# Performance work log

Hardware: AMD Instinct MI355X
Metric: run time of the kernel (lower is better)

## Reference

```python
import jax, jax.numpy as jnp
import numpy as np

GAMMAK = 1.0 / 256.0  # 1/(2*d) so kernel values don't underflow for unit-gaussian data


def setup_inputs() -> dict:
    key = jax.random.key(0)
    k1, k2, k3, k4, k5 = jax.random.split(key, 5)
    N, d = 8192, 128
    X = jax.random.normal(k1, (N, d), dtype=jnp.float32)
    y = jax.random.normal(k2, (N - 1, d), dtype=jnp.float32)
    y_next = jax.random.normal(k3, (N - 1, d), dtype=jnp.float32)
    # reset_transform initializes R=eye, t=0; perturb slightly for nontrivial math
    R = jnp.eye(d, dtype=jnp.float32) + 0.01 * jax.random.normal(k4, (d, d), dtype=jnp.float32)
    t = 0.01 * jax.random.normal(k5, (d, 1), dtype=jnp.float32)
    return {"X": X, "y": y, "y_next": y_next, "R": R, "t": t}


def reference(X, y, y_next, R, t):
    # _transform_pts: (R @ y.T + t).T == y @ R.T + t.squeeze()
    yt = y @ R.T + t[:, 0]            # (N-1, d)
    Xb = X[:-1]                        # (N-1, d) kernel base points
    # pairwise_sqeuclidean(Xb, yt), clamped at 0
    sq = jnp.clip(
        jnp.sum(Xb * Xb, axis=1)[:, None]
        + jnp.sum(yt * yt, axis=1)[None, :]
        - 2.0 * (Xb @ yt.T),
        0.0, None,
    )                                  # (N-1, N-1)
    G = jnp.exp(-GAMMAK * sq)
    # diag(1/rowsum) @ G  ==  G / rowsum[:, None]  (avoids explicit NxN diagonal)
    y_pred = (G / jnp.sum(G, axis=1, keepdims=True)) @ X[1:]  # (N-1, d)
    return y_pred
```

## Files before the change

### kernel.cpp

```cpp
#include <hip/hip_runtime.h>
#include <hip/hip_bf16.h>


#define LOG2E 1.44269504088896340736f
#define KNEG (-(1.0f/256.0f)*LOG2E)
#define KA2C (2.0f*(1.0f/256.0f)*LOG2E)

typedef __attribute__((ext_vector_type(4)))  float f32x4;
typedef __attribute__((ext_vector_type(16))) float f32x16;
typedef __attribute__((ext_vector_type(8)))  short bf16x8;

__device__ __forceinline__ unsigned short f2bf(float f) {
  unsigned u = __builtin_bit_cast(unsigned, f);
  u = (u + 0x7fffu + ((u >> 16) & 1u)) >> 16;
  return (unsigned short)u;
}
__device__ __forceinline__ unsigned pk2bf(float a, float b) {
  __hip_bfloat162 h = __float22bfloat162_rn(float2{a, b});
  unsigned u;
  __builtin_memcpy(&u, &h, 4);
  return u;
}
__device__ __forceinline__ bf16x8 pack8(float4 p0, float4 p1) {
  uint4 u;
  u.x = pk2bf(p0.x, p0.y); u.y = pk2bf(p0.z, p0.w);
  u.z = pk2bf(p1.x, p1.y); u.w = pk2bf(p1.z, p1.w);
  return __builtin_bit_cast(bf16x8, u);
}
__device__ __forceinline__ float fast_exp2(float x) {
#if __has_builtin(__builtin_amdgcn_exp2f)
  return __builtin_amdgcn_exp2f(x);
#else
  return exp2f(x);
#endif
}
__device__ __forceinline__ void gl2lds16(const void* g, void* l) {
  __builtin_amdgcn_global_load_lds((const __attribute__((address_space(1))) unsigned int*)g,
                                   (__attribute__((address_space(3))) unsigned int*)l, 16, 0, 0);
}
__device__ __forceinline__ f32x16 mfma_32x32x16(bf16x8 a, bf16x8 b, f32x16 c) {
  return __builtin_amdgcn_mfma_f32_32x32x16_bf16(a, b, c, 0, 0, 0);
}

#define T_STRIDE 34816
#define V_OFF    18432

__global__ __launch_bounds__(256) void k_prep(const float* __restrict__ y,
                                              const float* __restrict__ R,
                                              const float* __restrict__ t,
                                              const float* __restrict__ X,
                                              unsigned short* __restrict__ ctp) {
  __shared__ union {
    struct { unsigned short ytt[128 * 132]; float ynl[128]; } yb;
    float xt[65 * 132];
  } sm;
  const int tid = threadIdx.x;

  if (blockIdx.x < 64) {
    const int wv = tid >> 6, ln = tid & 63;
    const int l = ln & 31, h = ln >> 5;
    const int B = blockIdx.x;
    const int rw = B * 128 + wv * 32;

    bf16x8 af[8];
    {
      int row = rw + l; if (row > 8190) row = 8190;
      const float* yr = y + (size_t)row * 128;
#pragma unroll
      for (int kc = 0; kc < 8; ++kc) {
        float4 p0 = *(const float4*)(yr + kc*16 + 8*h);
        float4 p1 = *(const float4*)(yr + kc*16 + 8*h + 4);
        af[kc] = pack8(p0, p1);
      }
    }
    f32x16 acc[4];
#pragma unroll
    for (int cc=0; cc<4; ++cc)
#pragma unroll
      for (int i=0;i<16;++i) acc[cc][i] = 0.f;
#pragma unroll
    for (int cc=0; cc<4; ++cc) {
      const float* Rr = R + (size_t)(cc*32 + l) * 128;
#pragma unroll
      for (int kc=0; kc<8; ++kc) {
        float4 p0 = *(const float4*)(Rr + kc*16 + 8*h);
        float4 p1 = *(const float4*)(Rr + kc*16 + 8*h + 4);
        acc[cc] = mfma_32x32x16(af[kc], pack8(p0, p1), acc[cc]);
      }
    }
    float tv0 = t[l], tv1 = t[32+l], tv2 = t[64+l], tv3 = t[96+l];
    float v0[16], v1[16], v2[16], v3[16], ssq[16];
#pragma unroll
    for (int r=0;r<16;++r) {
      v0[r]=acc[0][r]+tv0; v1[r]=acc[1][r]+tv1; v2[r]=acc[2][r]+tv2; v3[r]=acc[3][r]+tv3;
      ssq[r] = v0[r]*v0[r] + v1[r]*v1[r] + v2[r]*v2[r] + v3[r]*v3[r];
    }
#pragma unroll
    for (int off=1; off<32; off<<=1)
#pragma unroll
      for (int r=0;r<16;++r) ssq[r] += __shfl_xor(ssq[r], off, 64);
    if (l < 16) {
      int r = l;
      int rloc = wv*32 + (r&3) + 8*(r>>2) + 4*h;
      int grow = rw + (r&3) + 8*(r>>2) + 4*h;
      sm.yb.ynl[rloc] = (grow >= 8191) ? -1.0e4f : KNEG * ssq[r];
    }
#pragma unroll
    for (int r=0;r<16;++r) {
      int rloc = wv*32 + (r&3) + 8*(r>>2) + 4*h;
      sm.yb.ytt[rloc*132 +   0 + l] = f2bf(KA2C * v0[r]);
      sm.yb.ytt[rloc*132 +  32 + l] = f2bf(KA2C * v1[r]);
      sm.yb.ytt[rloc*132 +  64 + l] = f2bf(KA2C * v2[r]);
      sm.yb.ytt[rloc*132 +  96 + l] = f2bf(KA2C * v3[r]);
    }
    __syncthreads();
    const int Tt = B*2 + (wv>>1);
    const int jcw = wv & 1;
    char* base = (char*)ctp + (size_t)Tt*T_STRIDE;
#pragma unroll
    for (int kc=0;kc<8;++kc) {
      const unsigned short* s = &sm.yb.ytt[(wv*32 + l)*132 + kc*16 + 8*h];
      uint2 a = *(const uint2*)(s);
      uint2 b = *(const uint2*)(s + 4);
      uint4 o; o.x=a.x; o.y=a.y; o.z=b.x; o.w=b.y;
      *(uint4*)(base + (jcw*9 + kc)*1024 + ln*16) = o;
    }
    {
      float yn = sm.yb.ynl[wv*32 + l];
      unsigned short hi = f2bf(yn);
      float hif = __builtin_bit_cast(float, (unsigned)hi << 16);
      unsigned short lo = f2bf(yn - hif);
      uint4 o; o.x = (h == 0) ? ((unsigned)hi | ((unsigned)lo << 16)) : 0u;
      o.y = 0u; o.z = 0u; o.w = 0u;
      *(uint4*)(base + (jcw*9 + 8)*1024 + ln*16) = o;
    }
  } else {
    const int T = blockIdx.x - 64;
    const int jt = T * 64;
    {
      int rr = tid >> 2, q4 = tid & 3;
      int row = jt + rr; if (row > 8191) row = 8191;
      const float* src = X + (size_t)row*128 + q4*32;
      float* dst = &sm.xt[rr*132 + q4*32];
#pragma unroll
      for (int i=0;i<8;++i) *(float4*)(dst + i*4) = *(const float4*)(src + i*4);
      if (tid < 4) {
        int row2 = jt + 64; if (row2 > 8191) row2 = 8191;
        const float* s2 = X + (size_t)row2*128 + tid*32;
        float* d2 = &sm.xt[64*132 + tid*32];
#pragma unroll
        for (int i=0;i<8;++i) *(float4*)(d2 + i*4) = *(const float4*)(s2 + i*4);
      }
    }
    __syncthreads();
    char* base = (char*)ctp + (size_t)T*T_STRIDE + V_OFF;
#pragma unroll
    for (int it=0; it<4; ++it) {
      int E = tid + it*256;
      int lp = E & 63, grp = E >> 6;
      int cc = grp & 3, jc16 = grp >> 2;
      int jb = jc16*16 + 8*(lp>>5);
      int c  = cc*32 + (lp & 31);
      uint4 o;
      o.x = pk2bf(sm.xt[(jb+1)*132 + c], sm.xt[(jb+2)*132 + c]);
      o.y = pk2bf(sm.xt[(jb+3)*132 + c], sm.xt[(jb+4)*132 + c]);
      o.z = pk2bf(sm.xt[(jb+5)*132 + c], sm.xt[(jb+6)*132 + c]);
      o.w = pk2bf(sm.xt[(jb+7)*132 + c], sm.xt[(jb+8)*132 + c]);
      *(uint4*)(base + E*16) = o;
    }
  }
}

__global__ __launch_bounds__(256, 3) void k_main(
    const float* __restrict__ X,
    const unsigned short* __restrict__ ctp,
    float* __restrict__ accp,
    float* __restrict__ rsp,
    int js) {
  __shared__ unsigned short stg[T_STRIDE/2];
  __shared__ unsigned short gls[4*32*68];
  const int tid = threadIdx.x;
  const int wv = tid >> 6, ln = tid & 63;
  const int l = ln & 31, h = ln >> 5;
  const int row = blockIdx.x*128 + wv*32 + l;

  bf16x8 qf[9];
  {
    const float* xr = X + (size_t)row * 128;
#pragma unroll
    for (int kc=0;kc<8;++kc) {
      float4 p0 = *(const float4*)(xr + kc*16 + 8*h);
      float4 p1 = *(const float4*)(xr + kc*16 + 8*h + 4);
      qf[kc] = pack8(p0, p1);
    }
    uint4 o; o.x = (h == 0) ? 0x3F803F80u : 0u; o.y = 0u; o.z = 0u; o.w = 0u;
    qf[8] = __builtin_bit_cast(bf16x8, o);
  }
  f32x16 acc[4];
#pragma unroll
  for (int cc=0;cc<4;++cc)
#pragma unroll
    for (int i=0;i<16;++i) acc[cc][i]=0.f;
  float rs = 0.f;
  const int sp = blockIdx.y;
  const int Tbeg = (sp * 128) / js;
  const int Tend = ((sp + 1) * 128) / js;
  for (int T = Tbeg; T < Tend; ++T) {
    __syncthreads();
    {
      const char* cb = (const char*)ctp + (size_t)T*T_STRIDE;
#pragma unroll
      for (int i=0;i<9;++i) {
        int c = wv + 4*i;
        if (c < 34) gl2lds16(cb + c*1024 + ln*16, (char*)stg + c*1024);
      }
    }
    __syncthreads();
#pragma unroll
    for (int jc=0; jc<2; ++jc) {
      f32x16 sa;
#pragma unroll
      for (int i=0;i<16;++i) sa[i]=0.f;
#pragma unroll
      for (int kc=0;kc<9;++kc) {
        bf16x8 a = *(const bf16x8*)((const char*)stg + (jc*9+kc)*1024 + ln*16);
        sa = mfma_32x32x16(a, qf[kc], sa);
      }
#pragma unroll
      for (int rg=0; rg<4; ++rg) {
        float g0 = fast_exp2(sa[rg*4+0]);
        float g1 = fast_exp2(sa[rg*4+1]);
        float g2 = fast_exp2(sa[rg*4+2]);
        float g3 = fast_exp2(sa[rg*4+3]);
        rs += (g0+g1) + (g2+g3);
        uint2 w; w.x = pk2bf(g0, g1); w.y = pk2bf(g2, g3);
        int j0 = jc*32 + 8*rg + 4*h;
        *(uint2*)&gls[(wv*32+l)*68 + j0] = w;
      }
      __builtin_amdgcn_wave_barrier();
#pragma unroll
      for (int jj=0; jj<2; ++jj) {
        int jc16 = jc*2 + jj;
        const unsigned short* gp = &gls[(wv*32+l)*68 + jc16*16 + 8*h];
        uint2 g0 = *(const uint2*)(gp);
        uint2 g1 = *(const uint2*)(gp + 4);
        uint4 gv; gv.x=g0.x; gv.y=g0.y; gv.z=g1.x; gv.w=g1.y;
        bf16x8 pb = __builtin_bit_cast(bf16x8, gv);
#pragma unroll
        for (int cc=0;cc<4;++cc) {
          bf16x8 a2 = *(const bf16x8*)((const char*)stg + V_OFF + (jc16*4+cc)*1024 + ln*16);
          acc[cc] = mfma_32x32x16(a2, pb, acc[cc]);
        }
      }
      __builtin_amdgcn_wave_barrier();
    }
  }
  rs += __shfl_xor(rs, 32, 64);
  if (h == 0) rsp[(size_t)sp*8192 + row] = rs;
#pragma unroll
  for (int cc=0;cc<4;++cc)
#pragma unroll
    for (int r=0;r<16;++r) {
      int c = cc*32 + (r&3) + 8*(r>>2) + 4*h;
      accp[((size_t)sp*128 + c)*8192 + row] = acc[cc][r];
    }
}

__global__ __launch_bounds__(256) void k_fin(const float* __restrict__ accp,
                                             const float* __restrict__ rsp,
                                             float* __restrict__ out,
                                             int js) {
  __shared__ float tr[64*132];
  __shared__ float rinv[64];
  const int tid = threadIdx.x;
  const int r0 = blockIdx.x * 64;
  if (tid < 64) {
    float s = 0.f;
    for (int sp=0; sp<js; ++sp) s += rsp[(size_t)sp*8192 + r0 + tid];
    rinv[tid] = 1.f / s;
  }
  const int rq = tid & 15, cg = tid >> 4;
  float v[8][4];
#pragma unroll
  for (int cc=0;cc<8;++cc)
#pragma unroll
    for (int k=0;k<4;++k) v[cc][k]=0.f;
  for (int sp=0; sp<js; ++sp) {
    const float* base = accp + ((size_t)sp*128 + cg*8)*8192 + r0 + rq*4;
#pragma unroll
    for (int cc=0; cc<8; ++cc) {
      float4 p = *(const float4*)(base + (size_t)cc*8192);
      v[cc][0]+=p.x; v[cc][1]+=p.y; v[cc][2]+=p.z; v[cc][3]+=p.w;
    }
  }
  __syncthreads();
#pragma unroll
  for (int cc=0;cc<8;++cc)
#pragma unroll
    for (int k=0;k<4;++k)
      tr[(rq*4+k)*132 + cg*8+cc] = v[cc][k] * rinv[rq*4+k];
  __syncthreads();
  {
    int r = tid >> 2, q = tid & 3;
    int grow = r0 + r;
    if (grow < 8191) {
      float* dst = out + (size_t)grow*128 + q*32;
      const float* s2 = &tr[r*132 + q*32];
#pragma unroll
      for (int i=0;i<8;++i) *(float4*)(dst + i*4) = *(const float4*)(s2 + i*4);
    }
  }
}

extern "C" void kernel_launch(void* const* d_in, const int* in_sizes, int n_in,
                              void* d_out, int out_size, void* d_ws, size_t ws_size,
                              hipStream_t stream) {
  const float* X = (const float*)d_in[0];
  const float* y = (const float*)d_in[1];
  const float* R = (const float*)d_in[3];
  const float* t = (const float*)d_in[4];
  float* out = (float*)d_out;
  char* ws = (char*)d_ws;

  unsigned short* ctp = (unsigned short*)ws;
  size_t rspoff = (size_t)128 * T_STRIDE;
  float* rsp  = (float*)(ws + rspoff);
  size_t accoff = rspoff + 512*1024;
  float* accp = (float*)(ws + accoff);

  int js = 12;
  while (js > 1 && accoff + (size_t)js*128*8192*4 > ws_size) js >>= 1;

  k_prep<<<dim3(192), dim3(256), 0, stream>>>(y, R, t, X, ctp);
  k_main<<<dim3(64, js), dim3(256), 0, stream>>>(X, ctp, accp, rsp, js);
  k_fin<<<dim3(128), dim3(256), 0, stream>>>(accp, rsp, out, js);
}
```

Measured before the change: 140.3 us.

## Double-buffer LDS tiles, add y-norm in fp32, shuffle P instead of LDS

The y-norm term no longer rides along as a ninth bf16 hi/lo K-chunk in the score MFMA. It now goes to a separate fp32 array and is added before exp2, which cuts one MFMA per chunk and removes a precision workaround. The per-tile global-to-LDS copy becomes double-buffered so the next tile loads while the current one computes. The exp'd probabilities are reshuffled across half-waves with cross-lane shuffles rather than a round trip through an LDS scratch buffer. Occupancy drops from 3 to 2 blocks because of the larger LDS, the split count changes from 12 to 8, and the finalize kernel is split across two column halves.

```diff
diff --git a/kernel.cpp b/kernel.cpp
--- a/kernel.cpp
+++ b/kernel.cpp
@@ -42,16 +42,17 @@
   return __builtin_amdgcn_mfma_f32_32x32x16_bf16(a, b, c, 0, 0, 0);
 }
 
-#define T_STRIDE 34816
-#define V_OFF    18432
+#define T_STRIDE 32768
+#define V_OFF    16384
 
 __global__ __launch_bounds__(256) void k_prep(const float* __restrict__ y,
                                               const float* __restrict__ R,
                                               const float* __restrict__ t,
                                               const float* __restrict__ X,
-                                              unsigned short* __restrict__ ctp) {
+                                              unsigned short* __restrict__ ctp,
+                                              float* __restrict__ ynp) {
   __shared__ union {
-    struct { unsigned short ytt[128 * 132]; float ynl[128]; } yb;
+    unsigned short ytt[128 * 132];
     float xt[65 * 132];
   } sm;
   const int tid = threadIdx.x;
@@ -101,17 +102,16 @@
       for (int r=0;r<16;++r) ssq[r] += __shfl_xor(ssq[r], off, 64);
     if (l < 16) {
       int r = l;
-      int rloc = wv*32 + (r&3) + 8*(r>>2) + 4*h;
       int grow = rw + (r&3) + 8*(r>>2) + 4*h;
-      sm.yb.ynl[rloc] = (grow >= 8191) ? -1.0e4f : KNEG * ssq[r];
+      ynp[grow] = (grow >= 8191) ? -1.0e30f : KNEG * ssq[r];
     }
 #pragma unroll
     for (int r=0;r<16;++r) {
       int rloc = wv*32 + (r&3) + 8*(r>>2) + 4*h;
-      sm.yb.ytt[rloc*132 +   0 + l] = f2bf(KA2C * v0[r]);
-      sm.yb.ytt[rloc*132 +  32 + l] = f2bf(KA2C * v1[r]);
-      sm.yb.ytt[rloc*132 +  64 + l] = f2bf(KA2C * v2[r]);
-      sm.yb.ytt[rloc*132 +  96 + l] = f2bf(KA2C * v3[r]);
+      sm.ytt[rloc*132 +   0 + l] = f2bf(KA2C * v0[r]);
+      sm.ytt[rloc*132 +  32 + l] = f2bf(KA2C * v1[r]);
+      sm.ytt[rloc*132 +  64 + l] = f2bf(KA2C * v2[r]);
+      sm.ytt[rloc*132 +  96 + l] = f2bf(KA2C * v3[r]);
     }
     __syncthreads();
     const int Tt = B*2 + (wv>>1);
@@ -119,20 +119,11 @@
     char* base = (char*)ctp + (size_t)Tt*T_STRIDE;
 #pragma unroll
     for (int kc=0;kc<8;++kc) {
-      const unsigned short* s = &sm.yb.ytt[(wv*32 + l)*132 + kc*16 + 8*h];
+      const unsigned short* s = &sm.ytt[(wv*32 + l)*132 + kc*16 + 8*h];
       uint2 a = *(const uint2*)(s);
       uint2 b = *(const uint2*)(s + 4);
       uint4 o; o.x=a.x; o.y=a.y; o.z=b.x; o.w=b.y;
-      *(uint4*)(base + (jcw*9 + kc)*1024 + ln*16) = o;
-    }
-    {
-      float yn = sm.yb.ynl[wv*32 + l];
-      unsigned short hi = f2bf(yn);
-      float hif = __builtin_bit_cast(float, (unsigned)hi << 16);
-      unsigned short lo = f2bf(yn - hif);
-      uint4 o; o.x = (h == 0) ? ((unsigned)hi | ((unsigned)lo << 16)) : 0u;
-      o.y = 0u; o.z = 0u; o.w = 0u;
-      *(uint4*)(base + (jcw*9 + 8)*1024 + ln*16) = o;
+      *(uint4*)(base + (jcw*8 + kc)*1024 + ln*16) = o;
     }
   } else {
     const int T = blockIdx.x - 64;
@@ -171,20 +162,20 @@
   }
 }
 
-__global__ __launch_bounds__(256, 3) void k_main(
+__global__ __launch_bounds__(256, 2) void k_main(
     const float* __restrict__ X,
     const unsigned short* __restrict__ ctp,
+    const float* __restrict__ ynp,
     float* __restrict__ accp,
     float* __restrict__ rsp,
     int js) {
-  __shared__ unsigned short stg[T_STRIDE/2];
-  __shared__ unsigned short gls[4*32*68];
+  __shared__ unsigned short stg[2][T_STRIDE/2];
   const int tid = threadIdx.x;
   const int wv = tid >> 6, ln = tid & 63;
   const int l = ln & 31, h = ln >> 5;
   const int row = blockIdx.x*128 + wv*32 + l;
 
-  bf16x8 qf[9];
+  bf16x8 qf[8];
   {
     const float* xr = X + (size_t)row * 128;
 #pragma unroll
@@ -193,8 +184,6 @@
       float4 p1 = *(const float4*)(xr + kc*16 + 8*h + 4);
       qf[kc] = pack8(p0, p1);
     }
-    uint4 o; o.x = (h == 0) ? 0x3F803F80u : 0u; o.y = 0u; o.z = 0u; o.w = 0u;
-    qf[8] = __builtin_bit_cast(bf16x8, o);
   }
   f32x16 acc[4];
 #pragma unroll
@@ -205,55 +194,80 @@
   const int sp = blockIdx.y;
   const int Tbeg = (sp * 128) / js;
   const int Tend = ((sp + 1) * 128) / js;
+
+  {
+    const char* cb = (const char*)ctp + (size_t)Tbeg*T_STRIDE;
+#pragma unroll
+    for (int i=0;i<8;++i) {
+      int c = wv + 4*i;
+      gl2lds16(cb + c*1024 + ln*16, (char*)stg[0] + c*1024);
+    }
+  }
+  int cur = 0;
   for (int T = Tbeg; T < Tend; ++T) {
     __syncthreads();
-    {
-      const char* cb = (const char*)ctp + (size_t)T*T_STRIDE;
-#pragma unroll
-      for (int i=0;i<9;++i) {
+    if (T + 1 < Tend) {
+      const char* cb = (const char*)ctp + (size_t)(T+1)*T_STRIDE;
+#pragma unroll
+      for (int i=0;i<8;++i) {
         int c = wv + 4*i;
-        if (c < 34) gl2lds16(cb + c*1024 + ln*16, (char*)stg + c*1024);
-      }
-    }
-    __syncthreads();
-#pragma unroll
-    for (int jc=0; jc<2; ++jc) {
-      f32x16 sa;
-#pragma unroll
-      for (int i=0;i<16;++i) sa[i]=0.f;
-#pragma unroll
-      for (int kc=0;kc<9;++kc) {
-        bf16x8 a = *(const bf16x8*)((const char*)stg + (jc*9+kc)*1024 + ln*16);
-        sa = mfma_32x32x16(a, qf[kc], sa);
-      }
-#pragma unroll
-      for (int rg=0; rg<4; ++rg) {
-        float g0 = fast_exp2(sa[rg*4+0]);
-        float g1 = fast_exp2(sa[rg*4+1]);
-        float g2 = fast_exp2(sa[rg*4+2]);
-        float g3 = fast_exp2(sa[rg*4+3]);
-        rs += (g0+g1) + (g2+g3);
-        uint2 w; w.x = pk2bf(g0, g1); w.y = pk2bf(g2, g3);
-        int j0 = jc*32 + 8*rg + 4*h;
-        *(uint2*)&gls[(wv*32+l)*68 + j0] = w;
-      }
-      __builtin_amdgcn_wave_barrier();
-#pragma unroll
-      for (int jj=0; jj<2; ++jj) {
-        int jc16 = jc*2 + jj;
-        const unsigned short* gp = &gls[(wv*32+l)*68 + jc16*16 + 8*h];
-        uint2 g0 = *(const uint2*)(gp);
-        uint2 g1 = *(const uint2*)(gp + 4);
-        uint4 gv; gv.x=g0.x; gv.y=g0.y; gv.z=g1.x; gv.w=g1.y;
-        bf16x8 pb = __builtin_bit_cast(bf16x8, gv);
+        gl2lds16(cb + c*1024 + ln*16, (char*)stg[cur^1] + c*1024);
+      }
+    }
+    const char* yb = (const char*)stg[cur];
+    const char* vb = (const char*)stg[cur] + V_OFF;
+    f32x4 yv[2][4];
+#pragma unroll
+    for (int jc=0;jc<2;++jc)
+#pragma unroll
+      for (int rg=0;rg<4;++rg)
+        yv[jc][rg] = *(const f32x4*)(ynp + T*64 + jc*32 + 8*rg + 4*h);
+    f32x16 sa[2];
+#pragma unroll
+    for (int jc=0;jc<2;++jc) {
+#pragma unroll
+      for (int i=0;i<16;++i) sa[jc][i]=0.f;
+#pragma unroll
+      for (int kc=0;kc<8;++kc) {
+        bf16x8 a = *(const bf16x8*)(yb + (jc*8+kc)*1024 + ln*16);
+        sa[jc] = mfma_32x32x16(a, qf[kc], sa[jc]);
+      }
+    }
+#pragma unroll
+    for (int jc=0;jc<2;++jc) {
+      float gg[16];
+#pragma unroll
+      for (int rg=0;rg<4;++rg) {
+#pragma unroll
+        for (int i=0;i<4;++i) {
+          float g = fast_exp2(sa[jc][rg*4+i] + yv[jc][rg][i]);
+          gg[rg*4+i] = g;
+          rs += g;
+        }
+      }
+#pragma unroll
+      for (int b=0;b<2;++b) {
+        unsigned own0 = pk2bf(gg[8*b+4*h+0], gg[8*b+4*h+1]);
+        unsigned own1 = pk2bf(gg[8*b+4*h+2], gg[8*b+4*h+3]);
+        unsigned snd0 = pk2bf(gg[8*b+4-4*h+0], gg[8*b+4-4*h+1]);
+        unsigned snd1 = pk2bf(gg[8*b+4-4*h+2], gg[8*b+4-4*h+3]);
+        unsigned rcv0 = (unsigned)__shfl_xor((int)snd0, 32, 64);
+        unsigned rcv1 = (unsigned)__shfl_xor((int)snd1, 32, 64);
+        uint4 u;
+        u.x = h ? rcv0 : own0;
+        u.y = h ? rcv1 : own1;
+        u.z = h ? own0 : rcv0;
+        u.w = h ? own1 : rcv1;
+        bf16x8 pb = __builtin_bit_cast(bf16x8, u);
+        int jc16 = jc*2 + b;
 #pragma unroll
         for (int cc=0;cc<4;++cc) {
-          bf16x8 a2 = *(const bf16x8*)((const char*)stg + V_OFF + (jc16*4+cc)*1024 + ln*16);
+          bf16x8 a2 = *(const bf16x8*)(vb + (jc16*4+cc)*1024 + ln*16);
           acc[cc] = mfma_32x32x16(a2, pb, acc[cc]);
         }
       }
-      __builtin_amdgcn_wave_barrier();
-    }
+    }
+    cur ^= 1;
   }
   rs += __shfl_xor(rs, 32, 64);
   if (h == 0) rsp[(size_t)sp*8192 + row] = rs;
@@ -270,44 +284,45 @@
                                              const float* __restrict__ rsp,
                                              float* __restrict__ out,
                                              int js) {
-  __shared__ float tr[64*132];
+  __shared__ float tr[64*68];
   __shared__ float rinv[64];
   const int tid = threadIdx.x;
   const int r0 = blockIdx.x * 64;
+  const int c0 = blockIdx.y * 64;
   if (tid < 64) {
     float s = 0.f;
     for (int sp=0; sp<js; ++sp) s += rsp[(size_t)sp*8192 + r0 + tid];
     rinv[tid] = 1.f / s;
   }
   const int rq = tid & 15, cg = tid >> 4;
-  float v[8][4];
-#pragma unroll
-  for (int cc=0;cc<8;++cc)
+  float v[4][4];
+#pragma unroll
+  for (int cc=0;cc<4;++cc)
 #pragma unroll
     for (int k=0;k<4;++k) v[cc][k]=0.f;
   for (int sp=0; sp<js; ++sp) {
-    const float* base = accp + ((size_t)sp*128 + cg*8)*8192 + r0 + rq*4;
-#pragma unroll
-    for (int cc=0; cc<8; ++cc) {
+    const float* base = accp + ((size_t)sp*128 + c0 + cg*4)*8192 + r0 + rq*4;
+#pragma unroll
+    for (int cc=0; cc<4; ++cc) {
       float4 p = *(const float4*)(base + (size_t)cc*8192);
       v[cc][0]+=p.x; v[cc][1]+=p.y; v[cc][2]+=p.z; v[cc][3]+=p.w;
     }
   }
   __syncthreads();
 #pragma unroll
-  for (int cc=0;cc<8;++cc)
+  for (int cc=0;cc<4;++cc)
 #pragma unroll
     for (int k=0;k<4;++k)
-      tr[(rq*4+k)*132 + cg*8+cc] = v[cc][k] * rinv[rq*4+k];
+      tr[(rq*4+k)*68 + cg*4+cc] = v[cc][k] * rinv[rq*4+k];
   __syncthreads();
   {
     int r = tid >> 2, q = tid & 3;
     int grow = r0 + r;
     if (grow < 8191) {
-      float* dst = out + (size_t)grow*128 + q*32;
-      const float* s2 = &tr[r*132 + q*32];
-#pragma unroll
-      for (int i=0;i<8;++i) *(float4*)(dst + i*4) = *(const float4*)(s2 + i*4);
+      float* dst = out + (size_t)grow*128 + c0 + q*16;
+      const float* s2 = &tr[r*68 + q*16];
+#pragma unroll
+      for (int i=0;i<4;++i) *(float4*)(dst + i*4) = *(const float4*)(s2 + i*4);
     }
   }
 }
@@ -323,15 +338,17 @@
   char* ws = (char*)d_ws;
 
   unsigned short* ctp = (unsigned short*)ws;
-  size_t rspoff = (size_t)128 * T_STRIDE;
+  size_t ynoff = (size_t)128 * T_STRIDE;
+  float* ynp = (float*)(ws + ynoff);
+  size_t rspoff = ynoff + 32*1024;
   float* rsp  = (float*)(ws + rspoff);
   size_t accoff = rspoff + 512*1024;
   float* accp = (float*)(ws + accoff);
 
-  int js = 12;
+  int js = 8;
   while (js > 1 && accoff + (size_t)js*128*8192*4 > ws_size) js >>= 1;
 
-  k_prep<<<dim3(192), dim3(256), 0, stream>>>(y, R, t, X, ctp);
-  k_main<<<dim3(64, js), dim3(256), 0, stream>>>(X, ctp, accp, rsp, js);
-  k_fin<<<dim3(128), dim3(256), 0, stream>>>(accp, rsp, out, js);
-}
+  k_prep<<<dim3(192), dim3(256), 0, stream>>>(y, R, t, X, ctp, ynp);
+  k_main<<<dim3(64, js), dim3(256), 0, stream>>>(X, ctp, ynp, accp, rsp, js);
+  k_fin<<<dim3(128, 2), dim3(256), 0, stream>>>(accp, rsp, out, js);
+}
```

New measurement: 170.2 us. 1.21x slower.
